# Performance work log

Hardware: AMD Instinct MI355X
Metric: run time of the kernel (lower is better)

Reference implementation:

```python
import jax, jax.numpy as jnp
import numpy as np
from jax import lax

N_FILTERS = 256
N_ITER = 20
N_HISTORY = 4
N_CLASSES = 100
BITS = 8            # n_bits_activ passed to Quan_layer
POOL_FREQ = 5
EPS = 1e-5


def quantize_ste(w, bits):
    # Uniform symmetric quantization to `bits` with straight-through estimator.
    n = 2.0 ** (bits - 1) - 1.0
    s = jnp.max(jnp.abs(w)) / n
    q = jnp.round(w / s) * s
    return w + lax.stop_gradient(q - w)


def max_pool2(x):
    return lax.reduce_window(x, -jnp.inf, lax.max, (1, 1, 2, 2), (1, 1, 2, 2), 'VALID')


def setup_inputs() -> dict:
    key = jax.random.key(0)
    ks = jax.random.split(key, 5)
    x = jax.random.normal(ks[0], (16, 3, 64, 64), jnp.float32)
    conv_w = jax.random.normal(ks[1], (N_FILTERS, N_FILTERS, 3, 3), jnp.float32) / np.sqrt(9.0 * N_FILTERS).astype(np.float32)
    alpha = jnp.zeros((N_ITER, N_HISTORY + 1), jnp.float32)
    alpha = alpha.at[:, 0].set(0.1).at[:, 1].set(0.9)
    alpha = alpha + 0.01 * jax.random.normal(ks[2], (N_ITER, N_HISTORY + 1), jnp.float32)
    bn_gamma = jnp.ones((N_ITER, N_FILTERS), jnp.float32)
    bn_beta = jnp.zeros((N_ITER, N_FILTERS), jnp.float32)
    out_w = jax.random.normal(ks[3], (N_CLASSES, N_FILTERS), jnp.float32) / np.sqrt(float(N_FILTERS)).astype(np.float32)
    out_b = jnp.zeros((N_CLASSES,), jnp.float32)
    return {'x': x, 'conv_w': conv_w, 'alpha': alpha, 'bn_gamma': bn_gamma,
            'bn_beta': bn_beta, 'out_w': out_w, 'out_b': out_b}


def reference(x, conv_w, alpha, bn_gamma, bn_beta, out_w, out_b):
    pool_at = [t % POOL_FREQ == POOL_FREQ - 1 for t in range(N_ITER)]
    c_in = x.shape[1]
    # zero-pad channels up to n_filters (F.pad on dim 1)
    x = jnp.pad(x, ((0, 0), (0, N_FILTERS - c_in), (0, 0), (0, 0)))
    hist = [None] * (N_HISTORY - 1) + [x]
    wq = quantize_ste(conv_w, BITS)  # shared quantized conv weight
    for t in range(N_ITER):
        a = lax.conv_general_dilated(hist[-1], wq, (1, 1), ((1, 1), (1, 1)),
                                     dimension_numbers=('NCHW', 'OIHW', 'NCHW'))
        a = jax.nn.relu(a)
        a = alpha[t, 0] * a
        for i, h in enumerate(hist):
            if h is not None:
                a = a + alpha[t, i + 1] * h
        # BatchNorm2d (training-mode batch stats, biased variance)
        mean = jnp.mean(a, axis=(0, 2, 3), keepdims=True)
        var = jnp.var(a, axis=(0, 2, 3), keepdims=True)
        a = (a - mean) / jnp.sqrt(var + EPS)
        a = a * bn_gamma[t][None, :, None, None] + bn_beta[t][None, :, None, None]
        # faithful shift: hist[0] is never overwritten (stays None)
        hist = [hist[0]] + hist[2:] + [a]
        if pool_at[t]:
            hist = [None if h is None else max_pool2(h) for h in hist]
    out = jnp.max(hist[-1], axis=(2, 3))  # adaptive_max_pool2d -> (1,1)
    return out @ out_w.T + out_b
```

## Files before the change

### kernel.cpp

```cpp
#include <hip/hip_runtime.h>
#include <hip/hip_fp16.h>
#include <cstddef>
#include <cstdint>


#define NB 16
#define NIT 20

typedef _Float16 half8 __attribute__((ext_vector_type(8)));
typedef _Float16 half4v __attribute__((ext_vector_type(4)));
typedef float floatx4 __attribute__((ext_vector_type(4)));

__device__ __forceinline__ void gl_lds16(const void* g, void* l) {
  __builtin_amdgcn_global_load_lds(
      (const __attribute__((address_space(1))) unsigned int*)g,
      (__attribute__((address_space(3))) unsigned int*)l, 16, 0, 0);
}

template <int N>
__device__ __forceinline__ void wait_vm() {
  if constexpr (N == 0) asm volatile("s_waitcnt vmcnt(0)" ::: "memory");
  else if constexpr (N == 5) asm volatile("s_waitcnt vmcnt(5)" ::: "memory");
  else if constexpr (N == 6) asm volatile("s_waitcnt vmcnt(6)" ::: "memory");
  else static_assert(N == 0 || N == 5 || N == 6, "add vmcnt literal");
}

__global__ void wmax_part_kernel(const float* __restrict__ w, float* __restrict__ part, int n) {
  float m = 0.f;
  for (int i = blockIdx.x * blockDim.x + threadIdx.x; i < n; i += gridDim.x * blockDim.x)
    m = fmaxf(m, fabsf(w[i]));
  #pragma unroll
  for (int o = 32; o > 0; o >>= 1) m = fmaxf(m, __shfl_down(m, o));
  __shared__ float sm[4];
  int wid = threadIdx.x >> 6, lane = threadIdx.x & 63;
  if (lane == 0) sm[wid] = m;
  __syncthreads();
  if (threadIdx.x == 0) part[blockIdx.x] = fmaxf(fmaxf(sm[0], sm[1]), fmaxf(sm[2], sm[3]));
}

__global__ void wmax_final_kernel(const float* __restrict__ part, float* __restrict__ sout) {
  float m = part[threadIdx.x];
  #pragma unroll
  for (int o = 32; o > 0; o >>= 1) m = fmaxf(m, __shfl_down(m, o));
  __shared__ float sm[4];
  int wid = threadIdx.x >> 6, lane = threadIdx.x & 63;
  if (lane == 0) sm[wid] = m;
  __syncthreads();
  if (threadIdx.x == 0) sout[0] = fmaxf(fmaxf(sm[0], sm[1]), fmaxf(sm[2], sm[3])) / 127.f;
}

__global__ void quant_kernel(const float* __restrict__ w, const float* __restrict__ sptr,
                             _Float16* __restrict__ wqr, int nw) {
  int d = blockIdx.x * 256 + threadIdx.x;
  if (d >= nw) return;
  int frag = d >> 9;
  int e = d & 511;
  int l = e >> 3, j = e & 7;
  int tap = frag >> 7;
  int rem = frag & 127;
  int cog = rem >> 3, chk = rem & 7;
  int co = cog * 16 + (l & 15);
  int ci = chk * 32 + (l >> 4) * 8 + j;
  float s = sptr[0];
  float q = rintf(w[((size_t)co * 256 + ci) * 9 + tap] / s) * s;
  wqr[d] = (_Float16)q;
}

__global__ void pad_kernel(const float* __restrict__ x, _Float16* __restrict__ out) {
  int idx = blockIdx.x * 256 + threadIdx.x;
  int c = idx & 255;
  int pos = idx >> 8;
  int hw = pos & 4095;
  int n = pos >> 12;
  float v = 0.f;
  if (c < 3) v = x[(n * 3 + c) * 4096 + hw];
  out[idx] = (_Float16)v;
}

template <int S, int R>
__global__ __launch_bounds__(512, 2) void conv_mfma_v7(
    const _Float16* __restrict__ in, const _Float16* __restrict__ wqr,
    const float* __restrict__ alpha, int t, int nc,
    const _Float16* h1, const _Float16* __restrict__ h2,
    const _Float16* __restrict__ h3, _Float16* pre,
    const _Float16* __restrict__ zpage,
    float* __restrict__ psum, float* __restrict__ psum2) {
  constexpr int NT = 512;
  constexpr int LW = S + 2;
  constexpr int XSLOT = (R + 2) * LW * 4;
  constexpr int XI = (XSLOT + NT - 1) / NT;
  constexpr int XPAD = XI * NT;
  constexpr int WSLOT = 36 * 64;
  constexpr int WI = (WSLOT + NT - 1) / NT;
  constexpr int WPAD = WI * NT;
  static_assert(R * S == 512, "block pixel tile must be 512");

  __shared__ half8 xl[2][XPAD];
  __shared__ half8 wl[WPAD];

  const int tid = threadIdx.x;
  const int lane = tid & 63;
  const int wid = tid >> 6;
  const int l16 = lane & 15;
  const int kg = lane >> 4;
  const int wn = wid;

  constexpr int BPI = S / R;
  const int n = blockIdx.x / BPI;
  const int rb = blockIdx.x % BPI;
  const int cob = blockIdx.y * 64;

  const _Float16* img = in + (size_t)n * S * S * 256;

  int rg[4], cg[4];
  #pragma unroll
  for (int g = 0; g < 4; ++g) {
    int lp = wn * 64 + g * 16 + l16;
    rg[g] = lp / S;
    cg[g] = lp - rg[g] * S;
  }

  floatx4 acc[4][4];
  #pragma unroll
  for (int f = 0; f < 4; ++f)
    #pragma unroll
    for (int g = 0; g < 4; ++g)
      acc[f][g] = (floatx4){0.f, 0.f, 0.f, 0.f};

  auto stageX = [&](int buf, int c) {
    const _Float16* cbase = img + c * 32;
    #pragma unroll
    for (int i = 0; i < XI; ++i) {
      int slot = i * NT + tid;
      const void* g = (const void*)zpage;
      if (slot < XSLOT) {
        int pix = slot >> 2;
        int cig = (slot & 3) ^ ((pix >> 1) & 3);
        int hp = pix / LW, wp = pix - hp * LW;
        int h = rb * R + hp - 1, w = wp - 1;
        if ((unsigned)h < (unsigned)S && (unsigned)w < (unsigned)S)
          g = (const void*)(cbase + (size_t)(h * S + w) * 256 + cig * 8);
      }
      gl_lds16(g, (void*)&xl[buf][slot]);
    }
  };

  auto stageW = [&](int c) {
    #pragma unroll
    for (int i = 0; i < WI; ++i) {
      int slot = i * NT + tid;
      const void* g = (const void*)zpage;
      if (slot < WSLOT) {
        int fb = slot >> 6;
        int tap = fb >> 2, f = fb & 3;
        int ll = slot & 63;
        g = (const void*)(wqr +
            ((((size_t)tap * 16 + blockIdx.y * 4 + f) * 8 + c) << 9) + ll * 8);
      }
      gl_lds16(g, (void*)&wl[slot]);
    }
  };

  auto compute = [&](const half8* xb) {
    #pragma unroll
    for (int tap = 0; tap < 9; ++tap) {
      const int dh = tap / 3 - 1;
      const int dw = tap - (tap / 3) * 3 - 1;
      half8 af[4];
      #pragma unroll
      for (int f = 0; f < 4; ++f)
        af[f] = wl[(tap * 4 + f) * 64 + lane];
      half8 bf[4];
      #pragma unroll
      for (int g = 0; g < 4; ++g) {
        int xp = (rg[g] + 1 + dh) * LW + (cg[g] + 1 + dw);
        bf[g] = xb[xp * 4 + (kg ^ ((xp >> 1) & 3))];
      }
      #pragma unroll
      for (int f = 0; f < 4; ++f)
        #pragma unroll
        for (int g = 0; g < 4; ++g)
          acc[f][g] = __builtin_amdgcn_mfma_f32_16x16x32_f16(af[f], bf[g], acc[f][g], 0, 0, 0);
    }
  };

  stageX(0, 0);
  stageW(0);
  wait_vm<0>();
  __builtin_amdgcn_sched_barrier(0);
  __builtin_amdgcn_s_barrier();
  __builtin_amdgcn_sched_barrier(0);

  for (int c = 0; c < nc; ++c) {
    if (c + 1 < nc) stageX((c + 1) & 1, c + 1);
    if (c > 0) {
      if (c + 1 < nc) wait_vm<XI>();
      else wait_vm<0>();
      __builtin_amdgcn_sched_barrier(0);
      __builtin_amdgcn_s_barrier();
      __builtin_amdgcn_sched_barrier(0);
    }
    compute(&xl[c & 1][0]);
    __builtin_amdgcn_sched_barrier(0);
    __builtin_amdgcn_s_barrier();
    __builtin_amdgcn_sched_barrier(0);
    if (c + 1 < nc) stageW(c + 1);
  }

  const float a0 = alpha[t * 5 + 0];
  const float a1 = alpha[t * 5 + 2];
  const float a2 = alpha[t * 5 + 3];
  const float a3 = alpha[t * 5 + 4];
  float cs[4][4], cq[4][4];
  #pragma unroll
  for (int f = 0; f < 4; ++f)
    #pragma unroll
    for (int r = 0; r < 4; ++r) { cs[f][r] = 0.f; cq[f][r] = 0.f; }

  const size_t pixbase = (size_t)n * S * S + (size_t)rb * (R * S);
  #pragma unroll
  for (int f = 0; f < 4; ++f) {
    const int co = cob + f * 16 + kg * 4;
    #pragma unroll
    for (int g = 0; g < 4; ++g) {
      int lp = wn * 64 + g * 16 + l16;
      size_t idx = (pixbase + lp) * 256 + co;
      half4v v3 = *(const half4v*)(h3 + idx);
      half4v v1 = {}, v2 = {};
      if (h1) v1 = *(const half4v*)(h1 + idx);
      if (h2) v2 = *(const half4v*)(h2 + idx);
      half4v o;
      #pragma unroll
      for (int r = 0; r < 4; ++r) {
        float pv = a0 * fmaxf(acc[f][g][r], 0.f) + a3 * (float)v3[r];
        if (h1) pv += a1 * (float)v1[r];
        if (h2) pv += a2 * (float)v2[r];
        o[r] = (_Float16)pv;
        cs[f][r] += pv;
        cq[f][r] += pv * pv;
      }
      *(half4v*)(pre + idx) = o;
    }
  }

  float* sred = reinterpret_cast<float*>(&wl[0]);
  #pragma unroll
  for (int f = 0; f < 4; ++f)
    #pragma unroll
    for (int r = 0; r < 4; ++r) {
      float a = cs[f][r], b = cq[f][r];
      #pragma unroll
      for (int m = 1; m < 16; m <<= 1) {
        a += __shfl_xor(a, m);
        b += __shfl_xor(b, m);
      }
      if (l16 == 0) {
        sred[wn * 64 + f * 16 + kg * 4 + r] = a;
        sred[512 + wn * 64 + f * 16 + kg * 4 + r] = b;
      }
    }
  __syncthreads();
  if (tid < 64) {
    float a = 0.f, b = 0.f;
    #pragma unroll
    for (int w = 0; w < 8; ++w) {
      a += sred[w * 64 + tid];
      b += sred[512 + w * 64 + tid];
    }
    psum[(size_t)blockIdx.x * 256 + cob + tid] = a;
    psum2[(size_t)blockIdx.x * 256 + cob + tid] = b;
  }
}

template <int S, int R>
__global__ __launch_bounds__(512, 2) void conv_mfma_sm(
    const _Float16* __restrict__ in, const _Float16* __restrict__ wqr,
    const float* __restrict__ alpha, int t,
    const _Float16* h1, const _Float16* __restrict__ h2,
    const _Float16* __restrict__ h3, _Float16* pre,
    const _Float16* __restrict__ zpage,
    float* __restrict__ psum, float* __restrict__ psum2) {
  constexpr int LW = S + 2;
  constexpr int PIX = (R + 2) * LW;
  constexpr int XS = PIX * 4;
  constexpr int XS_PAD = ((XS + 63) / 64) * 64;
  constexpr int WS = 36 * 64;
  constexpr int PIXB = R * S;
  constexpr int G = PIXB / 64;

  __shared__ half8 xl[2][XS_PAD];
  __shared__ half8 wl[2][WS];
  __shared__ float sred[8][4][2][4];
  __shared__ float sredq[8][4][2][4];

  const int tid = threadIdx.x;
  const int lane = tid & 63;
  const int wid = tid >> 6;
  const int l16 = lane & 15;
  const int kg = lane >> 4;
  const int wm = wid >> 2;
  const int wn = wid & 3;

  constexpr int BPI = S / R;
  const int n = blockIdx.x / BPI;
  const int rb = blockIdx.x % BPI;
  const int cob = blockIdx.y * 64;

  const _Float16* img = in + (size_t)n * S * S * 256;

  floatx4 acc[2][G];
  #pragma unroll
  for (int f = 0; f < 2; ++f)
    #pragma unroll
    for (int g = 0; g < G; ++g)
      acc[f][g] = (floatx4){0.f, 0.f, 0.f, 0.f};

  auto stage = [&](int buf, int c) {
    const _Float16* cbase = img + c * 32;
    for (int sb = wid * 64; sb < XS_PAD; sb += 512) {
      int slot = sb + lane;
      const void* g = (const void*)zpage;
      if (slot < XS) {
        int pix = slot >> 2;
        int cig = (slot & 3) ^ ((pix >> 1) & 3);
        int hp = pix / LW, wp = pix - hp * LW;
        int h = rb * R + hp - 1, w = wp - 1;
        if ((unsigned)h < (unsigned)S && (unsigned)w < (unsigned)S)
          g = (const void*)(cbase + (size_t)(h * S + w) * 256 + cig * 8);
      }
      gl_lds16(g, (void*)&xl[buf][sb]);
    }
    for (int fb = wid; fb < 36; fb += 8) {
      int tap = fb >> 2, cogl = fb & 3;
      const _Float16* g = wqr +
          ((((size_t)tap * 16 + blockIdx.y * 4 + cogl) * 8 + c) << 9) + lane * 8;
      gl_lds16((const void*)g, (void*)&wl[buf][fb * 64]);
    }
  };

  auto compute = [&](int buf) {
    #pragma unroll
    for (int dh = -1; dh <= 1; ++dh) {
      #pragma unroll
      for (int dw = -1; dw <= 1; ++dw) {
        const int tap = (dh + 1) * 3 + (dw + 1);
        half8 af[2];
        #pragma unroll
        for (int f = 0; f < 2; ++f)
          af[f] = wl[buf][(tap * 4 + wm * 2 + f) * 64 + lane];
        half8 bf[G];
        #pragma unroll
        for (int g = 0; g < G; ++g) {
          int p = wn * (PIXB / 4) + g * 16 + l16;
          int r = p / S, cc = p - r * S;
          int lp = (r + 1 + dh) * LW + (cc + 1 + dw);
          bf[g] = xl[buf][lp * 4 + (kg ^ ((lp >> 1) & 3))];
        }
        #pragma unroll
        for (int f = 0; f < 2; ++f)
          #pragma unroll
          for (int g = 0; g < G; ++g)
            acc[f][g] = __builtin_amdgcn_mfma_f32_16x16x32_f16(af[f], bf[g], acc[f][g], 0, 0, 0);
      }
    }
  };

  stage(0, 0);
  __syncthreads();
  for (int c = 0; c < 8; ++c) {
    if (c < 7) stage((c + 1) & 1, c + 1);
    compute(c & 1);
    __syncthreads();
  }

  const float a0 = alpha[t * 5 + 0];
  const float a1 = alpha[t * 5 + 2];
  const float a2 = alpha[t * 5 + 3];
  const float a3 = alpha[t * 5 + 4];
  float ss[2][4], sq[2][4];
  #pragma unroll
  for (int f = 0; f < 2; ++f)
    #pragma unroll
    for (int r = 0; r < 4; ++r) { ss[f][r] = 0.f; sq[f][r] = 0.f; }

  const size_t pix0 = (size_t)n * S * S + (size_t)rb * PIXB;
  #pragma unroll
  for (int f = 0; f < 2; ++f) {
    const int co = cob + wm * 32 + f * 16 + kg * 4;
    #pragma unroll
    for (int g = 0; g < G; ++g) {
      int p = wn * (PIXB / 4) + g * 16 + l16;
      size_t idx = (pix0 + p) * 256 + co;
      half4v v3 = *(const half4v*)(h3 + idx);
      half4v v1 = {}, v2 = {};
      if (h1) v1 = *(const half4v*)(h1 + idx);
      if (h2) v2 = *(const half4v*)(h2 + idx);
      half4v o;
      #pragma unroll
      for (int r = 0; r < 4; ++r) {
        float pv = a0 * fmaxf(acc[f][g][r], 0.f) + a3 * (float)v3[r];
        if (h1) pv += a1 * (float)v1[r];
        if (h2) pv += a2 * (float)v2[r];
        o[r] = (_Float16)pv;
        ss[f][r] += pv;
        sq[f][r] += pv * pv;
      }
      *(half4v*)(pre + idx) = o;
    }
  }

  #pragma unroll
  for (int f = 0; f < 2; ++f)
    #pragma unroll
    for (int r = 0; r < 4; ++r) {
      float a = ss[f][r], b = sq[f][r];
      #pragma unroll
      for (int m = 1; m < 16; m <<= 1) {
        a += __shfl_xor(a, m);
        b += __shfl_xor(b, m);
      }
      if (l16 == 0) { sred[wid][kg][f][r] = a; sredq[wid][kg][f][r] = b; }
    }
  __syncthreads();
  if (tid < 64) {
    int ch = tid;
    int wmm = ch >> 5, ff = (ch >> 4) & 1, kk = (ch >> 2) & 3, rr = ch & 3;
    float a = 0.f, b = 0.f;
    #pragma unroll
    for (int w = 0; w < 4; ++w) {
      a += sred[wmm * 4 + w][kk][ff][rr];
      b += sredq[wmm * 4 + w][kk][ff][rr];
    }
    psum[(size_t)blockIdx.x * 256 + cob + ch] = a;
    psum2[(size_t)blockIdx.x * 256 + cob + ch] = b;
  }
}

__global__ void stats_final_kernel(const float* __restrict__ psum, const float* __restrict__ psum2,
                                   const float* __restrict__ gamma, const float* __restrict__ beta,
                                   int t, float M, int nblk,
                                   float* __restrict__ scale, float* __restrict__ shift) {
  int c = blockIdx.x;
  float s = 0.f, s2 = 0.f;
  for (int b = threadIdx.x; b < nblk; b += 64) {
    s += psum[(size_t)b * 256 + c];
    s2 += psum2[(size_t)b * 256 + c];
  }
  #pragma unroll
  for (int o = 32; o > 0; o >>= 1) {
    s += __shfl_down(s, o);
    s2 += __shfl_down(s2, o);
  }
  if (threadIdx.x == 0) {
    float mean = s / M;
    float var = s2 / M - mean * mean;
    float sc = gamma[t * 256 + c] * rsqrtf(var + 1e-5f);
    scale[c] = sc;
    shift[c] = beta[t * 256 + c] - mean * sc;
  }
}

__global__ void apply_kernel(_Float16* __restrict__ x, const float* __restrict__ scale,
                             const float* __restrict__ shift, int n8) {
  int i = blockIdx.x * 256 + threadIdx.x;
  if (i >= n8) return;
  half8 v = *(half8*)(x + (size_t)i * 8);
  int c0 = (i * 8) & 255;
  half8 o;
  #pragma unroll
  for (int j = 0; j < 8; ++j) o[j] = (_Float16)((float)v[j] * scale[c0 + j] + shift[c0 + j]);
  *(half8*)(x + (size_t)i * 8) = o;
}

__global__ void pool3_kernel(const _Float16* __restrict__ s0, const _Float16* __restrict__ s1,
                             const _Float16* __restrict__ s2,
                             _Float16* __restrict__ d0, _Float16* __restrict__ d1,
                             _Float16* __restrict__ d2,
                             const float* __restrict__ scale, const float* __restrict__ shift,
                             int So, int total8) {
  int i = blockIdx.x * 256 + threadIdx.x;
  if (i >= total8) return;
  int z = blockIdx.y;
  const _Float16* in = (z == 0) ? s0 : (z == 1) ? s1 : s2;
  _Float16* out = (z == 0) ? d0 : (z == 1) ? d1 : d2;
  int c0 = (i & 31) * 8;
  int pix = i >> 5;
  int wo = pix % So;
  int t1 = pix / So;
  int ho = t1 % So;
  int n = t1 / So;
  int Si = So * 2;
  size_t b00 = ((size_t)(n * Si * Si) + (2 * ho) * Si + 2 * wo) * 256 + c0;
  half8 v00 = *(const half8*)(in + b00);
  half8 v01 = *(const half8*)(in + b00 + 256);
  half8 v10 = *(const half8*)(in + b00 + (size_t)Si * 256);
  half8 v11 = *(const half8*)(in + b00 + (size_t)Si * 256 + 256);
  half8 o;
  if (z == 2) {
    #pragma unroll
    for (int j = 0; j < 8; ++j) {
      float sc = scale[c0 + j], sh = shift[c0 + j];
      float a = (float)v00[j] * sc + sh;
      float b = (float)v01[j] * sc + sh;
      float c = (float)v10[j] * sc + sh;
      float d = (float)v11[j] * sc + sh;
      o[j] = (_Float16)fmaxf(fmaxf(a, b), fmaxf(c, d));
    }
  } else {
    #pragma unroll
    for (int j = 0; j < 8; ++j) {
      float m = fmaxf(fmaxf((float)v00[j], (float)v01[j]),
                      fmaxf((float)v10[j], (float)v11[j]));
      o[j] = (_Float16)m;
    }
  }
  *(half8*)(out + (size_t)pix * 256 + c0) = o;
}

__global__ void amax_kernel(const _Float16* __restrict__ x, float* __restrict__ vec) {
  int i = blockIdx.x * blockDim.x + threadIdx.x;
  if (i >= NB * 256) return;
  int n = i >> 8, c = i & 255;
  float m = -1e30f;
  for (int p = 0; p < 16; ++p)
    m = fmaxf(m, (float)x[((size_t)(n * 16 + p)) * 256 + c]);
  vec[i] = m;
}

__global__ void linear_kernel(const float* __restrict__ vec, const float* __restrict__ W,
                              const float* __restrict__ b, float* __restrict__ out) {
  int n = blockIdx.x, j = threadIdx.x;
  if (j >= 100) return;
  float s = b[j];
  const float* v = vec + n * 256;
  const float* w = W + j * 256;
  for (int c = 0; c < 256; ++c) s += v[c] * w[c];
  out[n * 100 + j] = s;
}

extern "C" void kernel_launch(void* const* d_in, const int* in_sizes, int n_in,
                              void* d_out, int out_size, void* d_ws, size_t ws_size,
                              hipStream_t stream) {
  const float* x        = (const float*)d_in[0];
  const float* conv_w   = (const float*)d_in[1];
  const float* alpha    = (const float*)d_in[2];
  const float* bn_gamma = (const float*)d_in[3];
  const float* bn_beta  = (const float*)d_in[4];
  const float* out_w    = (const float*)d_in[5];
  const float* out_b    = (const float*)d_in[6];
  float* out = (float*)d_out;

  char* ws = (char*)d_ws;
  size_t off = 0;
  auto alloc = [&](size_t bytes) -> void* {
    void* p = (void*)(ws + off);
    off = (off + bytes + 255) & ~(size_t)255;
    return p;
  };
  const size_t SLAB = (size_t)NB * 4096 * 256 * 2;
  char* slab[4];
  size_t slabsz[4];
  for (int i = 0; i < 3; ++i) { slab[i] = (char*)alloc(SLAB); slabsz[i] = SLAB; }
  slab[3] = (char*)alloc(3 * (SLAB / 4)); slabsz[3] = 3 * (SLAB / 4);
  _Float16* wqr  = (_Float16*)alloc((size_t)9 * 256 * 256 * 2);
  float* wpart = (float*)alloc(256 * 4);
  float* sq    = (float*)alloc(256);
  float* psum  = (float*)alloc(256 * 256 * 4);
  float* psum2 = (float*)alloc(256 * 256 * 4);
  float* scale = (float*)alloc(256 * 4);
  float* shift = (float*)alloc(256 * 4);
  float* vec   = (float*)alloc((size_t)NB * 256 * 4);
  _Float16* zpage = (_Float16*)alloc(256);
  (void)ws_size;

  const int NW = 256 * 256 * 9;

  hipMemsetAsync(zpage, 0, 256, stream);

  hipLaunchKernelGGL(wmax_part_kernel, dim3(256), dim3(256), 0, stream, conv_w, wpart, NW);
  hipLaunchKernelGGL(wmax_final_kernel, dim3(1), dim3(256), 0, stream, wpart, sq);
  hipLaunchKernelGGL(quant_kernel, dim3((NW + 255) / 256), dim3(256), 0, stream, conv_w, sq, wqr, NW);

  hipLaunchKernelGGL(pad_kernel, dim3((NB * 4096 * 256) / 256), dim3(256), 0, stream,
                     x, (_Float16*)slab[0]);

  auto contains = [&](int k, char* p) -> bool {
    return p && p >= slab[k] && p < slab[k] + slabsz[k];
  };

  char *p1 = nullptr, *p2 = nullptr, *p3 = slab[0];
  int S = 64;
  for (int t = 0; t < NIT; ++t) {
    char* dst;
    if (p1) {
      dst = p1;
    } else {
      dst = nullptr;
      for (int k = 0; k < 3; ++k)
        if (!contains(k, p2) && !contains(k, p3)) { dst = slab[k]; break; }
    }
    const _Float16* h1 = (const _Float16*)p1;
    const _Float16* h2 = (const _Float16*)p2;
    const _Float16* h3 = (const _Float16*)p3;
    _Float16* pre = (_Float16*)dst;

    int nblk;
    switch (S) {
      case 64: {
        int nc = (t == 0) ? 1 : 8;
        dim3 grid(NB * 8, 4);  nblk = NB * 8;
        hipLaunchKernelGGL((conv_mfma_v7<64, 8>), grid, dim3(512), 0, stream,
                           h3, wqr, alpha, t, nc, h1, h2, h3, pre, zpage, psum, psum2);
        break;
      }
      case 32: {
        dim3 grid(NB * 4, 4);  nblk = NB * 4;
        hipLaunchKernelGGL((conv_mfma_sm<32, 8>), grid, dim3(512), 0, stream,
                           h3, wqr, alpha, t, h1, h2, h3, pre, zpage, psum, psum2);
        break;
      }
      case 16: {
        dim3 grid(NB * 4, 4);  nblk = NB * 4;
        hipLaunchKernelGGL((conv_mfma_sm<16, 4>), grid, dim3(512), 0, stream,
                           h3, wqr, alpha, t, h1, h2, h3, pre, zpage, psum, psum2);
        break;
      }
      default: {
        dim3 grid(NB * 1, 4);  nblk = NB * 1;
        hipLaunchKernelGGL((conv_mfma_sm<8, 8>), grid, dim3(512), 0, stream,
                           h3, wqr, alpha, t, h1, h2, h3, pre, zpage, psum, psum2);
        break;
      }
    }

    int npix = NB * S * S;
    hipLaunchKernelGGL(stats_final_kernel, dim3(256), dim3(64), 0, stream,
                       psum, psum2, bn_gamma, bn_beta, t, (float)npix, nblk, scale, shift);

    if (t % 5 != 4) {
      int n8 = npix * 32;
      hipLaunchKernelGGL(apply_kernel, dim3((n8 + 255) / 256), dim3(256), 0, stream,
                         pre, scale, shift, n8);
      p1 = p2; p2 = p3; p3 = dst;
    } else {
      char* q1 = p2;
      char* q2 = p3;
      char* q3 = dst;
      int So = S / 2;
      size_t qbytes = (size_t)NB * So * So * 256 * 2;
      char* fs = nullptr;
      for (int k = 0; k < 4; ++k)
        if (!contains(k, q1) && !contains(k, q2) && !contains(k, q3)) { fs = slab[k]; break; }
      int total8 = NB * So * So * 32;
      dim3 pg((total8 + 255) / 256, 3);
      hipLaunchKernelGGL(pool3_kernel, pg, dim3(256), 0, stream,
                         (const _Float16*)q1, (const _Float16*)q2, (const _Float16*)q3,
                         (_Float16*)fs, (_Float16*)(fs + qbytes), (_Float16*)(fs + 2 * qbytes),
                         scale, shift, So, total8);
      p1 = fs; p2 = fs + qbytes; p3 = fs + 2 * qbytes;
      S = So;
    }
  }

  hipLaunchKernelGGL(amax_kernel, dim3(16), dim3(256), 0, stream, (const _Float16*)p3, vec);
  hipLaunchKernelGGL(linear_kernel, dim3(NB), dim3(128), 0, stream, vec, out_w, out_b, out);
}
```

Before: 1.031 ms.

## Fuse BN stats into apply/pool kernels, remap blocks across XCDs, merge small kernels

Folds the per-channel BN stats reduction into the apply and pool kernels. Each block recomputes scale and shift from the partial sums into LDS, which removes one launch per iteration. Also merges the weight-max final reduction into the quantize kernel and the amax and linear head into one kernel. Remaps conv block indices so the four output-channel groups of a pixel tile land on the same XCD for L2 reuse. The trade-off is that every block now redundantly reduces up to 256 partial rows, and grids become grid-stride loops capped at 512 blocks.

```diff
diff --git a/kernel.cpp b/kernel.cpp
--- a/kernel.cpp
+++ b/kernel.cpp
@@ -25,6 +25,13 @@
   else static_assert(N == 0 || N == 5 || N == 6, "add vmcnt literal");
 }
 
+__device__ __forceinline__ void xcd_remap(int ntile, int& tile, int& cog) {
+  int lin = blockIdx.y * gridDim.x + blockIdx.x;
+  cog = (lin >> 3) & 3;
+  tile = (lin & 7) + ((lin >> 5) << 3);
+  (void)ntile;
+}
+
 __global__ void wmax_part_kernel(const float* __restrict__ w, float* __restrict__ part, int n) {
   float m = 0.f;
   for (int i = blockIdx.x * blockDim.x + threadIdx.x; i < n; i += gridDim.x * blockDim.x)
@@ -38,19 +45,19 @@
   if (threadIdx.x == 0) part[blockIdx.x] = fmaxf(fmaxf(sm[0], sm[1]), fmaxf(sm[2], sm[3]));
 }
 
-__global__ void wmax_final_kernel(const float* __restrict__ part, float* __restrict__ sout) {
+__global__ void quant_kernel(const float* __restrict__ w, const float* __restrict__ part,
+                             _Float16* __restrict__ wqr, int nw) {
+  __shared__ float sm[4];
+  __shared__ float sS;
   float m = part[threadIdx.x];
   #pragma unroll
   for (int o = 32; o > 0; o >>= 1) m = fmaxf(m, __shfl_down(m, o));
-  __shared__ float sm[4];
   int wid = threadIdx.x >> 6, lane = threadIdx.x & 63;
   if (lane == 0) sm[wid] = m;
   __syncthreads();
-  if (threadIdx.x == 0) sout[0] = fmaxf(fmaxf(sm[0], sm[1]), fmaxf(sm[2], sm[3])) / 127.f;
-}
-
-__global__ void quant_kernel(const float* __restrict__ w, const float* __restrict__ sptr,
-                             _Float16* __restrict__ wqr, int nw) {
+  if (threadIdx.x == 0) sS = fmaxf(fmaxf(sm[0], sm[1]), fmaxf(sm[2], sm[3])) / 127.f;
+  __syncthreads();
+  float s = sS;
   int d = blockIdx.x * 256 + threadIdx.x;
   if (d >= nw) return;
   int frag = d >> 9;
@@ -61,7 +68,6 @@
   int cog = rem >> 3, chk = rem & 7;
   int co = cog * 16 + (l & 15);
   int ci = chk * 32 + (l >> 4) * 8 + j;
-  float s = sptr[0];
   float q = rintf(w[((size_t)co * 256 + ci) * 9 + tap] / s) * s;
   wqr[d] = (_Float16)q;
 }
@@ -106,9 +112,11 @@
   const int wn = wid;
 
   constexpr int BPI = S / R;
-  const int n = blockIdx.x / BPI;
-  const int rb = blockIdx.x % BPI;
-  const int cob = blockIdx.y * 64;
+  int tile, cog;
+  xcd_remap(NB * BPI, tile, cog);
+  const int n = tile / BPI;
+  const int rb = tile % BPI;
+  const int cob = cog * 64;
 
   const _Float16* img = in + (size_t)n * S * S * 256;
 
@@ -155,7 +163,7 @@
         int tap = fb >> 2, f = fb & 3;
         int ll = slot & 63;
         g = (const void*)(wqr +
-            ((((size_t)tap * 16 + blockIdx.y * 4 + f) * 8 + c) << 9) + ll * 8);
+            ((((size_t)tap * 16 + cog * 4 + f) * 8 + c) << 9) + ll * 8);
       }
       gl_lds16(g, (void*)&wl[slot]);
     }
@@ -267,8 +275,8 @@
       a += sred[w * 64 + tid];
       b += sred[512 + w * 64 + tid];
     }
-    psum[(size_t)blockIdx.x * 256 + cob + tid] = a;
-    psum2[(size_t)blockIdx.x * 256 + cob + tid] = b;
+    psum[(size_t)tile * 256 + cob + tid] = a;
+    psum2[(size_t)tile * 256 + cob + tid] = b;
   }
 }
 
@@ -302,9 +310,11 @@
   const int wn = wid & 3;
 
   constexpr int BPI = S / R;
-  const int n = blockIdx.x / BPI;
-  const int rb = blockIdx.x % BPI;
-  const int cob = blockIdx.y * 64;
+  int tile, cog;
+  xcd_remap(NB * BPI, tile, cog);
+  const int n = tile / BPI;
+  const int rb = tile % BPI;
+  const int cob = cog * 64;
 
   const _Float16* img = in + (size_t)n * S * S * 256;
 
@@ -333,7 +343,7 @@
     for (int fb = wid; fb < 36; fb += 8) {
       int tap = fb >> 2, cogl = fb & 3;
       const _Float16* g = wqr +
-          ((((size_t)tap * 16 + blockIdx.y * 4 + cogl) * 8 + c) << 9) + lane * 8;
+          ((((size_t)tap * 16 + cog * 4 + cogl) * 8 + c) << 9) + lane * 8;
       gl_lds16((const void*)g, (void*)&wl[buf][fb * 64]);
     }
   };
@@ -431,111 +441,117 @@
       a += sred[wmm * 4 + w][kk][ff][rr];
       b += sredq[wmm * 4 + w][kk][ff][rr];
     }
-    psum[(size_t)blockIdx.x * 256 + cob + ch] = a;
-    psum2[(size_t)blockIdx.x * 256 + cob + ch] = b;
-  }
-}
-
-__global__ void stats_final_kernel(const float* __restrict__ psum, const float* __restrict__ psum2,
-                                   const float* __restrict__ gamma, const float* __restrict__ beta,
-                                   int t, float M, int nblk,
-                                   float* __restrict__ scale, float* __restrict__ shift) {
-  int c = blockIdx.x;
-  float s = 0.f, s2 = 0.f;
-  for (int b = threadIdx.x; b < nblk; b += 64) {
-    s += psum[(size_t)b * 256 + c];
-    s2 += psum2[(size_t)b * 256 + c];
-  }
-  #pragma unroll
-  for (int o = 32; o > 0; o >>= 1) {
-    s += __shfl_down(s, o);
-    s2 += __shfl_down(s2, o);
-  }
-  if (threadIdx.x == 0) {
+    psum[(size_t)tile * 256 + cob + ch] = a;
+    psum2[(size_t)tile * 256 + cob + ch] = b;
+  }
+}
+
+__global__ __launch_bounds__(256) void bn_apply_fused(
+    _Float16* __restrict__ x, const float* __restrict__ psum,
+    const float* __restrict__ psum2, const float* __restrict__ gamma,
+    const float* __restrict__ beta, int t, float M, int nblk, int n8) {
+  __shared__ float ssc[256], ssh[256];
+  {
+    int c = threadIdx.x;
+    float s = 0.f, s2 = 0.f;
+    for (int b = 0; b < nblk; ++b) {
+      s += psum[(size_t)b * 256 + c];
+      s2 += psum2[(size_t)b * 256 + c];
+    }
     float mean = s / M;
     float var = s2 / M - mean * mean;
     float sc = gamma[t * 256 + c] * rsqrtf(var + 1e-5f);
-    scale[c] = sc;
-    shift[c] = beta[t * 256 + c] - mean * sc;
-  }
-}
-
-__global__ void apply_kernel(_Float16* __restrict__ x, const float* __restrict__ scale,
-                             const float* __restrict__ shift, int n8) {
-  int i = blockIdx.x * 256 + threadIdx.x;
-  if (i >= n8) return;
-  half8 v = *(half8*)(x + (size_t)i * 8);
-  int c0 = (i * 8) & 255;
-  half8 o;
-  #pragma unroll
-  for (int j = 0; j < 8; ++j) o[j] = (_Float16)((float)v[j] * scale[c0 + j] + shift[c0 + j]);
-  *(half8*)(x + (size_t)i * 8) = o;
-}
-
-__global__ void pool3_kernel(const _Float16* __restrict__ s0, const _Float16* __restrict__ s1,
-                             const _Float16* __restrict__ s2,
-                             _Float16* __restrict__ d0, _Float16* __restrict__ d1,
-                             _Float16* __restrict__ d2,
-                             const float* __restrict__ scale, const float* __restrict__ shift,
-                             int So, int total8) {
-  int i = blockIdx.x * 256 + threadIdx.x;
-  if (i >= total8) return;
+    ssc[c] = sc;
+    ssh[c] = beta[t * 256 + c] - mean * sc;
+  }
+  __syncthreads();
+  for (int i = blockIdx.x * 256 + threadIdx.x; i < n8; i += gridDim.x * 256) {
+    half8 v = *(half8*)(x + (size_t)i * 8);
+    int c0 = (i * 8) & 255;
+    half8 o;
+    #pragma unroll
+    for (int j = 0; j < 8; ++j) o[j] = (_Float16)((float)v[j] * ssc[c0 + j] + ssh[c0 + j]);
+    *(half8*)(x + (size_t)i * 8) = o;
+  }
+}
+
+__global__ __launch_bounds__(256) void pool3_kernel(
+    const _Float16* __restrict__ s0, const _Float16* __restrict__ s1,
+    const _Float16* __restrict__ s2,
+    _Float16* __restrict__ d0, _Float16* __restrict__ d1, _Float16* __restrict__ d2,
+    const float* __restrict__ psum, const float* __restrict__ psum2,
+    const float* __restrict__ gamma, const float* __restrict__ beta,
+    int t, float M, int nblk, int So, int total8) {
+  __shared__ float ssc[256], ssh[256];
   int z = blockIdx.y;
+  if (z == 2) {
+    int c = threadIdx.x;
+    float s = 0.f, s2 = 0.f;
+    for (int b = 0; b < nblk; ++b) {
+      s += psum[(size_t)b * 256 + c];
+      s2 += psum2[(size_t)b * 256 + c];
+    }
+    float mean = s / M;
+    float var = s2 / M - mean * mean;
+    float sc = gamma[t * 256 + c] * rsqrtf(var + 1e-5f);
+    ssc[c] = sc;
+    ssh[c] = beta[t * 256 + c] - mean * sc;
+    __syncthreads();
+  }
   const _Float16* in = (z == 0) ? s0 : (z == 1) ? s1 : s2;
   _Float16* out = (z == 0) ? d0 : (z == 1) ? d1 : d2;
-  int c0 = (i & 31) * 8;
-  int pix = i >> 5;
-  int wo = pix % So;
-  int t1 = pix / So;
-  int ho = t1 % So;
-  int n = t1 / So;
   int Si = So * 2;
-  size_t b00 = ((size_t)(n * Si * Si) + (2 * ho) * Si + 2 * wo) * 256 + c0;
-  half8 v00 = *(const half8*)(in + b00);
-  half8 v01 = *(const half8*)(in + b00 + 256);
-  half8 v10 = *(const half8*)(in + b00 + (size_t)Si * 256);
-  half8 v11 = *(const half8*)(in + b00 + (size_t)Si * 256 + 256);
-  half8 o;
-  if (z == 2) {
-    #pragma unroll
-    for (int j = 0; j < 8; ++j) {
-      float sc = scale[c0 + j], sh = shift[c0 + j];
-      float a = (float)v00[j] * sc + sh;
-      float b = (float)v01[j] * sc + sh;
-      float c = (float)v10[j] * sc + sh;
-      float d = (float)v11[j] * sc + sh;
-      o[j] = (_Float16)fmaxf(fmaxf(a, b), fmaxf(c, d));
-    }
-  } else {
-    #pragma unroll
-    for (int j = 0; j < 8; ++j) {
-      float m = fmaxf(fmaxf((float)v00[j], (float)v01[j]),
-                      fmaxf((float)v10[j], (float)v11[j]));
-      o[j] = (_Float16)m;
-    }
-  }
-  *(half8*)(out + (size_t)pix * 256 + c0) = o;
-}
-
-__global__ void amax_kernel(const _Float16* __restrict__ x, float* __restrict__ vec) {
-  int i = blockIdx.x * blockDim.x + threadIdx.x;
-  if (i >= NB * 256) return;
-  int n = i >> 8, c = i & 255;
+  for (int i = blockIdx.x * 256 + threadIdx.x; i < total8; i += gridDim.x * 256) {
+    int c0 = (i & 31) * 8;
+    int pix = i >> 5;
+    int wo = pix % So;
+    int t1 = pix / So;
+    int ho = t1 % So;
+    int n = t1 / So;
+    size_t b00 = ((size_t)(n * Si * Si) + (2 * ho) * Si + 2 * wo) * 256 + c0;
+    half8 v00 = *(const half8*)(in + b00);
+    half8 v01 = *(const half8*)(in + b00 + 256);
+    half8 v10 = *(const half8*)(in + b00 + (size_t)Si * 256);
+    half8 v11 = *(const half8*)(in + b00 + (size_t)Si * 256 + 256);
+    half8 o;
+    if (z == 2) {
+      #pragma unroll
+      for (int j = 0; j < 8; ++j) {
+        float sc = ssc[c0 + j], sh = ssh[c0 + j];
+        float a = (float)v00[j] * sc + sh;
+        float b = (float)v01[j] * sc + sh;
+        float c = (float)v10[j] * sc + sh;
+        float d = (float)v11[j] * sc + sh;
+        o[j] = (_Float16)fmaxf(fmaxf(a, b), fmaxf(c, d));
+      }
+    } else {
+      #pragma unroll
+      for (int j = 0; j < 8; ++j) {
+        float m = fmaxf(fmaxf((float)v00[j], (float)v01[j]),
+                        fmaxf((float)v10[j], (float)v11[j]));
+        o[j] = (_Float16)m;
+      }
+    }
+    *(half8*)(out + (size_t)pix * 256 + c0) = o;
+  }
+}
+
+__global__ __launch_bounds__(256) void head_kernel(
+    const _Float16* __restrict__ x, const float* __restrict__ W,
+    const float* __restrict__ b, float* __restrict__ out) {
+  __shared__ float v[256];
+  int n = blockIdx.x, c = threadIdx.x;
   float m = -1e30f;
   for (int p = 0; p < 16; ++p)
     m = fmaxf(m, (float)x[((size_t)(n * 16 + p)) * 256 + c]);
-  vec[i] = m;
-}
-
-__global__ void linear_kernel(const float* __restrict__ vec, const float* __restrict__ W,
-                              const float* __restrict__ b, float* __restrict__ out) {
-  int n = blockIdx.x, j = threadIdx.x;
-  if (j >= 100) return;
-  float s = b[j];
-  const float* v = vec + n * 256;
-  const float* w = W + j * 256;
-  for (int c = 0; c < 256; ++c) s += v[c] * w[c];
-  out[n * 100 + j] = s;
+  v[c] = m;
+  __syncthreads();
+  if (c < 100) {
+    float s = b[c];
+    const float* w = W + c * 256;
+    for (int k = 0; k < 256; ++k) s += v[k] * w[k];
+    out[n * 100 + c] = s;
+  }
 }
 
 extern "C" void kernel_launch(void* const* d_in, const int* in_sizes, int n_in,
@@ -564,12 +580,8 @@
   slab[3] = (char*)alloc(3 * (SLAB / 4)); slabsz[3] = 3 * (SLAB / 4);
   _Float16* wqr  = (_Float16*)alloc((size_t)9 * 256 * 256 * 2);
   float* wpart = (float*)alloc(256 * 4);
-  float* sq    = (float*)alloc(256);
   float* psum  = (float*)alloc(256 * 256 * 4);
   float* psum2 = (float*)alloc(256 * 256 * 4);
-  float* scale = (float*)alloc(256 * 4);
-  float* shift = (float*)alloc(256 * 4);
-  float* vec   = (float*)alloc((size_t)NB * 256 * 4);
   _Float16* zpage = (_Float16*)alloc(256);
   (void)ws_size;
 
@@ -578,8 +590,8 @@
   hipMemsetAsync(zpage, 0, 256, stream);
 
   hipLaunchKernelGGL(wmax_part_kernel, dim3(256), dim3(256), 0, stream, conv_w, wpart, NW);
-  hipLaunchKernelGGL(wmax_final_kernel, dim3(1), dim3(256), 0, stream, wpart, sq);
-  hipLaunchKernelGGL(quant_kernel, dim3((NW + 255) / 256), dim3(256), 0, stream, conv_w, sq, wqr, NW);
+  hipLaunchKernelGGL(quant_kernel, dim3((NW + 255) / 256), dim3(256), 0, stream,
+                     conv_w, wpart, wqr, NW);
 
   hipLaunchKernelGGL(pad_kernel, dim3((NB * 4096 * 256) / 256), dim3(256), 0, stream,
                      x, (_Float16*)slab[0]);
@@ -634,13 +646,13 @@
     }
 
     int npix = NB * S * S;
-    hipLaunchKernelGGL(stats_final_kernel, dim3(256), dim3(64), 0, stream,
-                       psum, psum2, bn_gamma, bn_beta, t, (float)npix, nblk, scale, shift);
 
     if (t % 5 != 4) {
       int n8 = npix * 32;
-      hipLaunchKernelGGL(apply_kernel, dim3((n8 + 255) / 256), dim3(256), 0, stream,
-                         pre, scale, shift, n8);
+      int blocks = (n8 + 255) / 256;
+      if (blocks > 512) blocks = 512;
+      hipLaunchKernelGGL(bn_apply_fused, dim3(blocks), dim3(256), 0, stream,
+                         pre, psum, psum2, bn_gamma, bn_beta, t, (float)npix, nblk, n8);
       p1 = p2; p2 = p3; p3 = dst;
     } else {
       char* q1 = p2;
@@ -652,16 +664,18 @@
       for (int k = 0; k < 4; ++k)
         if (!contains(k, q1) && !contains(k, q2) && !contains(k, q3)) { fs = slab[k]; break; }
       int total8 = NB * So * So * 32;
-      dim3 pg((total8 + 255) / 256, 3);
+      int pgx = (total8 + 255) / 256;
+      if (pgx > 512) pgx = 512;
+      dim3 pg(pgx, 3);
       hipLaunchKernelGGL(pool3_kernel, pg, dim3(256), 0, stream,
                          (const _Float16*)q1, (const _Float16*)q2, (const _Float16*)q3,
                          (_Float16*)fs, (_Float16*)(fs + qbytes), (_Float16*)(fs + 2 * qbytes),
-                         scale, shift, So, total8);
+                         psum, psum2, bn_gamma, bn_beta, t, (float)npix, nblk, So, total8);
       p1 = fs; p2 = fs + qbytes; p3 = fs + 2 * qbytes;
       S = So;
     }
   }
 
-  hipLaunchKernelGGL(amax_kernel, dim3(16), dim3(256), 0, stream, (const _Float16*)p3, vec);
-  hipLaunchKernelGGL(linear_kernel, dim3(NB), dim3(128), 0, stream, vec, out_w, out_b, out);
-}
+  hipLaunchKernelGGL(head_kernel, dim3(16), dim3(256), 0, stream,
+                     (const _Float16*)p3, out_w, out_b, out);
+}
```

Result: slower. 1.296 ms (+25.7%).
